# Optimization experiments

Measured on AMD Instinct MI355X. Metric: run time of the kernel, lower is better.

## Reference

```python
import jax, jax.numpy as jnp
import numpy as np

N_HEAD = 16
ROPE_BASE = 10000.0


def _rope_cos_sin(T, D, dtype):
    # D = head_size; matches RotaryEmbedding: emb = cat(freqs, freqs)
    inv_freq = 1.0 / (ROPE_BASE ** (jnp.arange(0, D, 2, dtype=jnp.float32) / D))
    t = jnp.arange(T, dtype=jnp.float32)
    freqs = t[:, None] * inv_freq[None, :]              # [T, D/2]
    emb = jnp.concatenate([freqs, freqs], axis=-1)      # [T, D]
    return jnp.cos(emb).astype(dtype), jnp.sin(emb).astype(dtype)


def _rotate_half(x):
    d = x.shape[-1] // 2
    return jnp.concatenate([-x[..., d:], x[..., :d]], axis=-1)


def setup_inputs() -> dict:
    key = jax.random.key(0)
    ks = jax.random.split(key, 5)
    B, T, C = 2, 2048, 1024
    s_in = 1.0 / np.sqrt(C)
    return {
        "x": jax.random.normal(ks[0], (B, T, C), dtype=jnp.float32),
        "w_attn": jax.random.normal(ks[1], (C, 3 * C), dtype=jnp.float32) * s_in,
        "b_attn": jnp.zeros((3 * C,), dtype=jnp.float32),
        "w_proj": jax.random.normal(ks[2], (C, C), dtype=jnp.float32) * s_in,
        "b_proj": jnp.zeros((C,), dtype=jnp.float32),
    }


def reference(x, w_attn, b_attn, w_proj, b_proj):
    B, T, C = x.shape
    H = N_HEAD
    D = C // H

    qkv = x @ w_attn + b_attn                            # [B,T,3C]
    q, k, v = jnp.split(qkv, 3, axis=-1)
    # [B,T,C] -> [B,H,T,D]
    to_heads = lambda a: a.reshape(B, T, H, D).transpose(0, 2, 1, 3)
    q, k, v = to_heads(q), to_heads(k), to_heads(v)

    cos, sin = _rope_cos_sin(T, D, x.dtype)              # [T,D] each, broadcast over B,H
    q = q * cos + _rotate_half(q) * sin
    k = k * cos + _rotate_half(k) * sin

    scale = 1.0 / np.sqrt(D)
    att = jnp.einsum("bhqd,bhkd->bhqk", q, k) * scale    # [B,H,T,T]
    causal = jnp.tril(jnp.ones((T, T), dtype=bool))
    att = jnp.where(causal, att, jnp.finfo(att.dtype).min)
    att = jax.nn.softmax(att, axis=-1)
    y = jnp.einsum("bhqk,bhkd->bhqd", att, v)            # [B,H,T,D]

    y = y.transpose(0, 2, 1, 3).reshape(B, T, C)
    return y @ w_proj + b_proj
```

## Files before the change

### kernel.cpp

```cpp
#include <hip/hip_runtime.h>
#include <hip/hip_bf16.h>

#define B_ 2
#define T_ 2048
#define C_ 1024
#define H_ 16
#define D_ 64

typedef __attribute__((ext_vector_type(8))) short bf16x8;
typedef __attribute__((ext_vector_type(4))) float f32x4;

static __device__ __forceinline__ float bf2f(unsigned short u) {
  union { unsigned int i; float f; } c;
  c.i = ((unsigned int)u) << 16;
  return c.f;
}
static __device__ __forceinline__ unsigned short f2bf(float f) {
  union { float f; unsigned int i; } c;
  c.f = f;
  unsigned int x = c.i;
  return (unsigned short)((x + 0x7fffu + ((x >> 16) & 1u)) >> 16);
}

static __device__ __forceinline__ void gl_lds16(const void* g, void* s) {
  __builtin_amdgcn_global_load_lds(
      (const __attribute__((address_space(1))) void*)g,
      (__attribute__((address_space(3))) void*)s, 16, 0, 0);
}

__global__ __launch_bounds__(256) void fill_kernel_f32(float* __restrict__ out,
                                                       int n, float v) {
  int i = blockIdx.x * 256 + threadIdx.x;
  if (i < n) out[i] = v;
}

__global__ __launch_bounds__(256) void prep_kernel(
    const float* __restrict__ w_attn, const float* __restrict__ w_proj,
    const float* __restrict__ x,
    unsigned short* __restrict__ waT, unsigned short* __restrict__ wpT,
    unsigned short* __restrict__ xb) {
  __shared__ float tile[32][33];
  const int z = blockIdx.z;
  if (z == 2) {
    const int id = blockIdx.y * 96 + blockIdx.x;
    if (id >= 2048) return;
    int i = (id * 256 + threadIdx.x) * 8;
    float4 f0 = *(const float4*)(x + i);
    float4 f1 = *(const float4*)(x + i + 4);
    union { unsigned short u[8]; uint4 v; } p;
    p.u[0] = f2bf(f0.x); p.u[1] = f2bf(f0.y); p.u[2] = f2bf(f0.z); p.u[3] = f2bf(f0.w);
    p.u[4] = f2bf(f1.x); p.u[5] = f2bf(f1.y); p.u[6] = f2bf(f1.z); p.u[7] = f2bf(f1.w);
    *(uint4*)(xb + i) = p.v;
    return;
  }
  const float* W;
  unsigned short* WT;
  int Kd, Nd;
  if (z == 0) { W = w_attn; WT = waT; Kd = 1024; Nd = 3072; }
  else {
    if (blockIdx.x >= 32) return;
    W = w_proj; WT = wpT; Kd = 1024; Nd = 1024;
  }
  const int n0 = blockIdx.x * 32, k0 = blockIdx.y * 32;
  const int tx = threadIdx.x & 31, ty = threadIdx.x >> 5;
#pragma unroll
  for (int i = 0; i < 4; ++i)
    tile[ty + i * 8][tx] = W[(size_t)(k0 + ty + i * 8) * Nd + n0 + tx];
  __syncthreads();
#pragma unroll
  for (int i = 0; i < 4; ++i)
    WT[(size_t)(n0 + ty + i * 8) * Kd + k0 + tx] = f2bf(tile[tx][ty + i * 8]);
}

template <int OUT_PLANES>
__global__ __launch_bounds__(256) void mfma_gemm(
    const unsigned short* __restrict__ A,
    const unsigned short* __restrict__ BT,
    const float* __restrict__ bias,
    unsigned short* __restrict__ qP, unsigned short* __restrict__ kP,
    unsigned short* __restrict__ vT, float* __restrict__ Fout,
    int N, int K) {
  __shared__ unsigned short S[128 * 128];
  unsigned short* As = S;
  unsigned short* Bs = S + 128 * 64;

  const int tid = threadIdx.x;
  const int w = tid >> 6, lane = tid & 63;
  const int lo = lane & 15, g = lane >> 4;
  const int wm = (w >> 1) * 64, wn = (w & 1) * 64;
  const int m0 = blockIdx.y * 128, n0 = blockIdx.x * 128;

  const int lr8 = lane >> 3;

  const f32x4 zero4 = {0.f, 0.f, 0.f, 0.f};
  f32x4 acc[4][4] = {{zero4, zero4, zero4, zero4}, {zero4, zero4, zero4, zero4},
                     {zero4, zero4, zero4, zero4}, {zero4, zero4, zero4, zero4}};

  for (int k0 = 0; k0 < K; k0 += 64) {
    __syncthreads();
#pragma unroll
    for (int it = 0; it < 4; ++it) {
      const int base_row = w * 32 + it * 8;
      const int r = base_row + lr8;
      const int j = (lane & 7) ^ (r & 7);
      gl_lds16(A + (size_t)(m0 + r) * K + k0 + j * 8, &As[base_row * 64]);
      gl_lds16(BT + (size_t)(n0 + r) * K + k0 + j * 8, &Bs[base_row * 64]);
    }
    __syncthreads();

#pragma unroll
    for (int kk = 0; kk < 2; ++kk) {
      bf16x8 af[4], bfr[4];
#pragma unroll
      for (int i = 0; i < 4; ++i) {
        int ra = wm + i * 16 + lo;
        int rb = wn + i * 16 + lo;
        af[i]  = *(const bf16x8*)&As[ra * 64 + ((g + kk * 4) ^ (ra & 7)) * 8];
        bfr[i] = *(const bf16x8*)&Bs[rb * 64 + ((g + kk * 4) ^ (rb & 7)) * 8];
      }
#pragma unroll
      for (int i = 0; i < 4; ++i)
#pragma unroll
        for (int j = 0; j < 4; ++j)
          acc[i][j] = __builtin_amdgcn_mfma_f32_16x16x32_bf16(af[i], bfr[j],
                                                              acc[i][j], 0, 0, 0);
    }
  }

  float bv[4];
#pragma unroll
  for (int j = 0; j < 4; ++j) bv[j] = bias[n0 + wn + j * 16 + lo];

  if (OUT_PLANES) {
    const int pl = n0 >> 10;
    if (pl == 2) {
      const int b = m0 >> 11;
      const int t0base = m0 & 2047;
      const int colbase = (n0 & 1023) + wn + lo;
#pragma unroll
      for (int i = 0; i < 4; ++i) {
        const int tt = t0base + wm + i * 16 + g * 4;
#pragma unroll
        for (int j = 0; j < 4; ++j) {
          const int col = colbase + j * 16;
          unsigned int u0 = (unsigned int)f2bf(acc[i][j][0] + bv[j]) |
                            ((unsigned int)f2bf(acc[i][j][1] + bv[j]) << 16);
          unsigned int u1 = (unsigned int)f2bf(acc[i][j][2] + bv[j]) |
                            ((unsigned int)f2bf(acc[i][j][3] + bv[j]) << 16);
          uint2 pw; pw.x = u0; pw.y = u1;
          *(uint2*)(vT + ((size_t)(b * 1024 + col)) * 2048 + tt) = pw;
        }
      }
    } else {
      __syncthreads();
      const float scale = (pl == 0) ? 0.125f : 1.0f;
      const float invA = exp2f((float)(-2 * lo) * (13.287712379549449f / 64.0f)) *
                         0.15915494309189535f;
      const float invB = exp2f((float)(-2 * (lo + 16)) * (13.287712379549449f / 64.0f)) *
                         0.15915494309189535f;
      const int c0 = wn + lo;
#pragma unroll
      for (int i = 0; i < 4; ++i)
#pragma unroll
        for (int r = 0; r < 4; ++r) {
          const int row = wm + i * 16 + g * 4 + r;
          const float t = (float)((m0 + row) & (T_ - 1));
          float ra = t * invA; ra -= floorf(ra);
          float rb = t * invB; rb -= floorf(rb);
          const float sA = __builtin_amdgcn_sinf(ra);
          const float cA = __builtin_amdgcn_cosf(ra);
          const float sB = __builtin_amdgcn_sinf(rb);
          const float cB = __builtin_amdgcn_cosf(rb);
          const float q1A = acc[i][0][r] + bv[0];
          const float q2A = acc[i][2][r] + bv[2];
          const float q1B = acc[i][1][r] + bv[1];
          const float q2B = acc[i][3][r] + bv[3];
          S[row * 128 + c0]      = f2bf((q1A * cA - q2A * sA) * scale);
          S[row * 128 + c0 + 32] = f2bf((q2A * cA + q1A * sA) * scale);
          S[row * 128 + c0 + 16] = f2bf((q1B * cB - q2B * sB) * scale);
          S[row * 128 + c0 + 48] = f2bf((q2B * cB + q1B * sB) * scale);
        }
      __syncthreads();
      unsigned short* P = (pl == 0) ? qP : kP;
      const int pcol0 = n0 & 1023;
#pragma unroll
      for (int it2 = 0; it2 < 8; ++it2) {
        const int p = it2 * 256 + tid;
        const int lrow = p >> 4;
        const int lcol = (p & 15) * 8;
        uint4 v4 = *(const uint4*)&S[lrow * 128 + lcol];
        *(uint4*)(P + (size_t)(m0 + lrow) * 1024 + pcol0 + lcol) = v4;
      }
    }
  } else {
    float* Sf = (float*)S;
#pragma unroll
    for (int hh = 0; hh < 2; ++hh) {
      __syncthreads();
      if ((w >> 1) == hh) {
#pragma unroll
        for (int i = 0; i < 4; ++i)
#pragma unroll
          for (int r = 0; r < 4; ++r) {
            const int lrow = i * 16 + g * 4 + r;
#pragma unroll
            for (int j = 0; j < 4; ++j)
              Sf[lrow * 128 + wn + j * 16 + lo] = acc[i][j][r] + bv[j];
          }
      }
      __syncthreads();
#pragma unroll
      for (int it2 = 0; it2 < 8; ++it2) {
        const int p = it2 * 256 + tid;
        const int lrow = p >> 5;
        const int lcol = (p & 31) * 4;
        float4 v4 = *(const float4*)&Sf[lrow * 128 + lcol];
        *(float4*)(Fout + (size_t)(m0 + hh * 64 + lrow) * N + n0 + lcol) = v4;
      }
    }
  }
}

__global__ __launch_bounds__(256) void flash_mfma6(
    unsigned short* __restrict__ qP,
    const unsigned short* __restrict__ kP,
    const unsigned short* __restrict__ vT) {
  const int cid = blockIdx.x;
  const int xcd = cid & 7;
  const int k6 = cid >> 3;
  const int bh = xcd * 4 + (k6 >> 4);
  const int bx = k6 & 15;
  const int b = bh >> 4, h = bh & 15;
  const int tid = threadIdx.x;
  const int w = tid >> 6, lane = tid & 63;
  const int lo = lane & 15, g = lane >> 4;

  __shared__ unsigned short Ks[64][72];
  __shared__ unsigned short VTs[64][72];
  __shared__ unsigned short Ps[64][72];

  const int srow = tid >> 3;
  const int sc8 = (tid & 7) * 8;
  const f32x4 zero4 = {0.f, 0.f, 0.f, 0.f};

#pragma unroll
  for (int half = 0; half < 2; ++half) {
    const int qt = half ? (31 - bx) : bx;
    const int rowq0 = b * T_ + qt * 64;

    const unsigned short* qrow = qP + (size_t)(rowq0 + w * 16 + lo) * 1024 + h * 64;
    bf16x8 aq0 = *(const bf16x8*)(qrow + g * 8);
    bf16x8 aq1 = *(const bf16x8*)(qrow + 32 + g * 8);

    f32x4 oacc[4] = {zero4, zero4, zero4, zero4};
    float lsum = 0.f;

    uint4 kreg0, kreg1, vreg0, vreg1;
    {
      const size_t kb = (size_t)(b * T_ + srow) * 1024 + h * 64 + sc8;
      kreg0 = *(const uint4*)(kP + kb);
      kreg1 = *(const uint4*)(kP + kb + (size_t)32 * 1024);
      const size_t vb = ((size_t)bh * 64 + srow) * 2048 + sc8;
      vreg0 = *(const uint4*)(vT + vb);
      vreg1 = *(const uint4*)(vT + vb + (size_t)32 * 2048);
    }

    for (int kt = 0; kt <= qt; ++kt) {
      __syncthreads();
      *(uint4*)&Ks[srow][sc8]       = kreg0;
      *(uint4*)&Ks[srow + 32][sc8]  = kreg1;
      *(uint4*)&VTs[srow][sc8]      = vreg0;
      *(uint4*)&VTs[srow + 32][sc8] = vreg1;
      __syncthreads();
      if (kt < qt) {
        const size_t kb = (size_t)(b * T_ + (kt + 1) * 64 + srow) * 1024 + h * 64 + sc8;
        kreg0 = *(const uint4*)(kP + kb);
        kreg1 = *(const uint4*)(kP + kb + (size_t)32 * 1024);
        const size_t vb = ((size_t)bh * 64 + srow) * 2048 + (kt + 1) * 64 + sc8;
        vreg0 = *(const uint4*)(vT + vb);
        vreg1 = *(const uint4*)(vT + vb + (size_t)32 * 2048);
      }

      f32x4 sacc[4] = {zero4, zero4, zero4, zero4};
      __builtin_amdgcn_s_setprio(1);
#pragma unroll
      for (int ct = 0; ct < 4; ++ct) {
        bf16x8 bk0 = *(const bf16x8*)&Ks[ct * 16 + lo][g * 8];
        bf16x8 bk1 = *(const bf16x8*)&Ks[ct * 16 + lo][32 + g * 8];
        sacc[ct] = __builtin_amdgcn_mfma_f32_16x16x32_bf16(bk0, aq0, sacc[ct], 0, 0, 0);
        sacc[ct] = __builtin_amdgcn_mfma_f32_16x16x32_bf16(bk1, aq1, sacc[ct], 0, 0, 0);
      }
      __builtin_amdgcn_s_setprio(0);

      if (kt == qt) {
#pragma unroll
        for (int ct = 0; ct < 4; ++ct)
#pragma unroll
          for (int r = 0; r < 4; ++r)
            if (ct * 16 + g * 4 + r > w * 16 + lo) sacc[ct][r] = -1e30f;
      }

#pragma unroll
      for (int ct = 0; ct < 4; ++ct) {
        float p0 = __expf(sacc[ct][0]);
        float p1 = __expf(sacc[ct][1]);
        float p2 = __expf(sacc[ct][2]);
        float p3 = __expf(sacc[ct][3]);
        lsum += (p0 + p1) + (p2 + p3);
        unsigned int u0 = (unsigned int)f2bf(p0) | ((unsigned int)f2bf(p1) << 16);
        unsigned int u1 = (unsigned int)f2bf(p2) | ((unsigned int)f2bf(p3) << 16);
        uint2 pw; pw.x = u0; pw.y = u1;
        *(uint2*)&Ps[w * 16 + lo][ct * 16 + g * 4] = pw;
      }

      bf16x8 ap0 = *(const bf16x8*)&Ps[w * 16 + lo][g * 8];
      bf16x8 ap1 = *(const bf16x8*)&Ps[w * 16 + lo][32 + g * 8];
      __builtin_amdgcn_s_setprio(1);
#pragma unroll
      for (int c2 = 0; c2 < 4; ++c2) {
        bf16x8 bv0 = *(const bf16x8*)&VTs[c2 * 16 + lo][g * 8];
        bf16x8 bv1 = *(const bf16x8*)&VTs[c2 * 16 + lo][32 + g * 8];
        oacc[c2] = __builtin_amdgcn_mfma_f32_16x16x32_bf16(ap0, bv0, oacc[c2], 0, 0, 0);
        oacc[c2] = __builtin_amdgcn_mfma_f32_16x16x32_bf16(ap1, bv1, oacc[c2], 0, 0, 0);
      }
      __builtin_amdgcn_s_setprio(0);
    }

    lsum += __shfl_xor(lsum, 16);
    lsum += __shfl_xor(lsum, 32);

#pragma unroll
    for (int r = 0; r < 4; ++r) {
      float inv_r = 1.0f / __shfl(lsum, g * 4 + r);
      unsigned short* dst = qP + (size_t)(rowq0 + w * 16 + g * 4 + r) * 1024 + h * 64 + lo;
#pragma unroll
      for (int c2 = 0; c2 < 4; ++c2)
        dst[c2 * 16] = f2bf(oacc[c2][r] * inv_r);
    }
  }
}

extern "C" void kernel_launch(void* const* d_in, const int* in_sizes, int n_in,
                              void* d_out, int out_size, void* d_ws, size_t ws_size,
                              hipStream_t stream) {
  const float *x = nullptr, *w_attn = nullptr, *b_attn = nullptr,
              *w_proj = nullptr, *b_proj = nullptr;
  for (int i = 0; i < n_in; ++i) {
    switch (in_sizes[i]) {
      case B_ * T_ * C_:  x      = (const float*)d_in[i]; break;
      case C_ * 3 * C_:   w_attn = (const float*)d_in[i]; break;
      case 3 * C_:        b_attn = (const float*)d_in[i]; break;
      case C_ * C_:       w_proj = (const float*)d_in[i]; break;
      case C_:            b_proj = (const float*)d_in[i]; break;
      default: break;
    }
  }
  float* out = (float*)d_out;
  const int nblk = (out_size + 255) / 256;

  if (!x || !w_attn || !b_attn || !w_proj || !b_proj) {
    fill_kernel_f32<<<nblk, 256, 0, stream>>>(out, out_size, 100.0f);
    return;
  }
  if (ws_size < (size_t)48 * 1024 * 1024) {
    fill_kernel_f32<<<nblk, 256, 0, stream>>>(out, out_size, 50.0f);
    return;
  }

  unsigned short* qP  = (unsigned short*)d_ws;
  unsigned short* kP  = qP + (size_t)(B_ * T_) * 1024;
  unsigned short* vP  = kP + (size_t)(B_ * T_) * 1024;
  unsigned short* vT  = vP + (size_t)(B_ * T_) * 1024;
  unsigned short* xb  = vT + (size_t)(B_ * T_) * 1024;
  unsigned short* waT = xb + (size_t)(B_ * T_) * C_;
  unsigned short* wpT = waT + (size_t)C_ * 3 * C_;
  (void)vP;

  prep_kernel<<<dim3(96, 32, 3), 256, 0, stream>>>(w_attn, w_proj, x, waT, wpT, xb);
  mfma_gemm<1><<<dim3((3 * C_) / 128, (B_ * T_) / 128), 256, 0, stream>>>(
      xb, waT, b_attn, qP, kP, vT, nullptr, 3 * C_, C_);
  flash_mfma6<<<dim3(512), 256, 0, stream>>>(qP, kP, vT);
  mfma_gemm<0><<<dim3(C_ / 128, (B_ * T_) / 128), 256, 0, stream>>>(
      qP, wpT, b_proj, nullptr, nullptr, nullptr, out, C_, C_);
}
```

Before: 183.6 us.

## Double-buffer flash K/V tiles with direct global-to-LDS loads and XOR swizzle

Replaces the register-staged K/V prefetch in the attention kernel with direct global-to-LDS async loads into double-buffered shared tiles. Bank conflicts are avoided with an XOR swizzle instead of padding. This removes the register round trip and one barrier per iteration, so the next tile's load can overlap compute. It doubles K/V LDS usage and relies on vmcnt waits being correct for the async LDS writes.

```diff
diff --git a/kernel.cpp b/kernel.cpp
--- a/kernel.cpp
+++ b/kernel.cpp
@@ -221,7 +221,21 @@
   }
 }
 
-__global__ __launch_bounds__(256) void flash_mfma6(
+static __device__ __forceinline__ void flash_stage(
+    const unsigned short* kbase, const unsigned short* vbase,
+    unsigned short* Kbuf, unsigned short* Vbuf,
+    int kt, int w, int lr8, int lc8) {
+#pragma unroll
+  for (int it = 0; it < 2; ++it) {
+    const int base = w * 16 + it * 8;
+    const int r = base + lr8;
+    const int j = lc8 ^ (r & 7);
+    gl_lds16(kbase + (size_t)(kt * 64 + r) * 1024 + j * 8, Kbuf + base * 64);
+    gl_lds16(vbase + (size_t)r * 2048 + kt * 64 + j * 8, Vbuf + base * 64);
+  }
+}
+
+__global__ __launch_bounds__(256) void flash_v14(
     unsigned short* __restrict__ qP,
     const unsigned short* __restrict__ kP,
     const unsigned short* __restrict__ vT) {
@@ -234,14 +248,16 @@
   const int tid = threadIdx.x;
   const int w = tid >> 6, lane = tid & 63;
   const int lo = lane & 15, g = lane >> 4;
-
-  __shared__ unsigned short Ks[64][72];
-  __shared__ unsigned short VTs[64][72];
+  const int lr8 = lane >> 3, lc8 = lane & 7;
+
+  __shared__ unsigned short Ks[2][64 * 64];
+  __shared__ unsigned short VTs[2][64 * 64];
   __shared__ unsigned short Ps[64][72];
 
-  const int srow = tid >> 3;
-  const int sc8 = (tid & 7) * 8;
   const f32x4 zero4 = {0.f, 0.f, 0.f, 0.f};
+
+  const unsigned short* kbase = kP + (size_t)b * T_ * 1024 + h * 64;
+  const unsigned short* vbase = vT + (size_t)bh * 64 * 2048;
 
 #pragma unroll
   for (int half = 0; half < 2; ++half) {
@@ -255,38 +271,23 @@
     f32x4 oacc[4] = {zero4, zero4, zero4, zero4};
     float lsum = 0.f;
 
-    uint4 kreg0, kreg1, vreg0, vreg1;
-    {
-      const size_t kb = (size_t)(b * T_ + srow) * 1024 + h * 64 + sc8;
-      kreg0 = *(const uint4*)(kP + kb);
-      kreg1 = *(const uint4*)(kP + kb + (size_t)32 * 1024);
-      const size_t vb = ((size_t)bh * 64 + srow) * 2048 + sc8;
-      vreg0 = *(const uint4*)(vT + vb);
-      vreg1 = *(const uint4*)(vT + vb + (size_t)32 * 2048);
-    }
+    flash_stage(kbase, vbase, Ks[0], VTs[0], 0, w, lr8, lc8);
+    asm volatile("s_waitcnt vmcnt(0)" ::: "memory");
+    __builtin_amdgcn_sched_barrier(0);
+    __builtin_amdgcn_s_barrier();
 
     for (int kt = 0; kt <= qt; ++kt) {
-      __syncthreads();
-      *(uint4*)&Ks[srow][sc8]       = kreg0;
-      *(uint4*)&Ks[srow + 32][sc8]  = kreg1;
-      *(uint4*)&VTs[srow][sc8]      = vreg0;
-      *(uint4*)&VTs[srow + 32][sc8] = vreg1;
-      __syncthreads();
-      if (kt < qt) {
-        const size_t kb = (size_t)(b * T_ + (kt + 1) * 64 + srow) * 1024 + h * 64 + sc8;
-        kreg0 = *(const uint4*)(kP + kb);
-        kreg1 = *(const uint4*)(kP + kb + (size_t)32 * 1024);
-        const size_t vb = ((size_t)bh * 64 + srow) * 2048 + (kt + 1) * 64 + sc8;
-        vreg0 = *(const uint4*)(vT + vb);
-        vreg1 = *(const uint4*)(vT + vb + (size_t)32 * 2048);
-      }
+      const int buf = kt & 1;
+      if (kt < qt)
+        flash_stage(kbase, vbase, Ks[buf ^ 1], VTs[buf ^ 1], kt + 1, w, lr8, lc8);
 
       f32x4 sacc[4] = {zero4, zero4, zero4, zero4};
       __builtin_amdgcn_s_setprio(1);
 #pragma unroll
       for (int ct = 0; ct < 4; ++ct) {
-        bf16x8 bk0 = *(const bf16x8*)&Ks[ct * 16 + lo][g * 8];
-        bf16x8 bk1 = *(const bf16x8*)&Ks[ct * 16 + lo][32 + g * 8];
+        const int r = ct * 16 + lo;
+        bf16x8 bk0 = *(const bf16x8*)&Ks[buf][r * 64 + ((g)     ^ (r & 7)) * 8];
+        bf16x8 bk1 = *(const bf16x8*)&Ks[buf][r * 64 + ((g + 4) ^ (r & 7)) * 8];
         sacc[ct] = __builtin_amdgcn_mfma_f32_16x16x32_bf16(bk0, aq0, sacc[ct], 0, 0, 0);
         sacc[ct] = __builtin_amdgcn_mfma_f32_16x16x32_bf16(bk1, aq1, sacc[ct], 0, 0, 0);
       }
@@ -318,12 +319,17 @@
       __builtin_amdgcn_s_setprio(1);
 #pragma unroll
       for (int c2 = 0; c2 < 4; ++c2) {
-        bf16x8 bv0 = *(const bf16x8*)&VTs[c2 * 16 + lo][g * 8];
-        bf16x8 bv1 = *(const bf16x8*)&VTs[c2 * 16 + lo][32 + g * 8];
+        const int r = c2 * 16 + lo;
+        bf16x8 bv0 = *(const bf16x8*)&VTs[buf][r * 64 + ((g)     ^ (r & 7)) * 8];
+        bf16x8 bv1 = *(const bf16x8*)&VTs[buf][r * 64 + ((g + 4) ^ (r & 7)) * 8];
         oacc[c2] = __builtin_amdgcn_mfma_f32_16x16x32_bf16(ap0, bv0, oacc[c2], 0, 0, 0);
         oacc[c2] = __builtin_amdgcn_mfma_f32_16x16x32_bf16(ap1, bv1, oacc[c2], 0, 0, 0);
       }
       __builtin_amdgcn_s_setprio(0);
+
+      asm volatile("s_waitcnt vmcnt(0)" ::: "memory");
+      __builtin_amdgcn_sched_barrier(0);
+      __builtin_amdgcn_s_barrier();
     }
 
     lsum += __shfl_xor(lsum, 16);
@@ -379,7 +385,7 @@
   prep_kernel<<<dim3(96, 32, 3), 256, 0, stream>>>(w_attn, w_proj, x, waT, wpT, xb);
   mfma_gemm<1><<<dim3((3 * C_) / 128, (B_ * T_) / 128), 256, 0, stream>>>(
       xb, waT, b_attn, qP, kP, vT, nullptr, 3 * C_, C_);
-  flash_mfma6<<<dim3(512), 256, 0, stream>>>(qP, kP, vT);
+  flash_v14<<<dim3(512), 256, 0, stream>>>(qP, kP, vT);
   mfma_gemm<0><<<dim3(C_ / 128, (B_ * T_) / 128), 256, 0, stream>>>(
       qP, wpT, b_proj, nullptr, nullptr, nullptr, out, C_, C_);
 }
```

After: 183.1 us. No clear change (-0.3%).
